# Optimization experiments

Hardware: AMD Instinct MI355X
Metric: run time of the kernel (lower is better)

Reference implementation:

```python
import jax, jax.numpy as jnp
import numpy as np

N = 50000
E = 800000
IN, HID, OUT = 20, 64, 2
HEADS, HD = 4, 64
EPS = 1e-5


def setup_inputs() -> dict:
    key = jax.random.key(0)
    ks = jax.random.split(key, 24)
    rn = lambda k, shape, s=0.1: (jax.random.normal(k, shape, dtype=jnp.float32) * s)
    inp = {}
    inp['x'] = jax.random.normal(ks[0], (N, IN), dtype=jnp.float32)
    inp['edge_index'] = jax.random.randint(ks[1], (2, E), 0, N, dtype=jnp.int64)
    # SAGEConv1: lin_l (aggregated msgs, bias), lin_r (root, no bias)
    inp['Wl1'] = rn(ks[2], (IN, HID)); inp['Wr1'] = rn(ks[3], (IN, HID)); inp['b1'] = jnp.zeros((HID,), jnp.float32)
    inp['g1'] = jnp.ones((HID,), jnp.float32); inp['bt1'] = jnp.zeros((HID,), jnp.float32)
    # GATConv: W2 projects to heads*dim; att vectors per head; bias size HID (concat=False)
    inp['W2'] = rn(ks[4], (HID, HEADS * HD)); inp['att_src'] = rn(ks[5], (HEADS, HD)); inp['att_dst'] = rn(ks[6], (HEADS, HD)); inp['b2'] = jnp.zeros((HID,), jnp.float32)
    inp['g2'] = jnp.ones((HID,), jnp.float32); inp['bt2'] = jnp.zeros((HID,), jnp.float32)
    # SAGEConv3: hidden -> hidden//2
    inp['Wl3'] = rn(ks[7], (HID, HID // 2)); inp['Wr3'] = rn(ks[8], (HID, HID // 2)); inp['b3'] = jnp.zeros((HID // 2,), jnp.float32)
    inp['g3'] = jnp.ones((HID // 2,), jnp.float32); inp['bt3'] = jnp.zeros((HID // 2,), jnp.float32)
    # skip + classifier
    inp['Wskip'] = rn(ks[9], (IN, HID // 2)); inp['bskip'] = jnp.zeros((HID // 2,), jnp.float32)
    inp['Wc1'] = rn(ks[10], (HID // 2, 32)); inp['bc1'] = jnp.zeros((32,), jnp.float32)
    inp['Wc2'] = rn(ks[11], (32, OUT)); inp['bc2'] = jnp.zeros((OUT,), jnp.float32)
    return inp


def _bn_eval(h, g, b):
    # eval-mode BatchNorm with freshly initialized running stats (mean=0, var=1)
    return h * (g / jnp.sqrt(1.0 + EPS)) + b


def reference(x, edge_index, Wl1, Wr1, b1, g1, bt1, W2, att_src, att_dst, b2, g2, bt2,
              Wl3, Wr3, b3, g3, bt3, Wskip, bskip, Wc1, bc1, Wc2, bc2):
    src, dst = edge_index[0], edge_index[1]
    deg = jnp.clip(jax.ops.segment_sum(jnp.ones((E,), x.dtype), dst, num_segments=N), 1.0)

    def sage(h, Wl, Wr, b):
        agg = jax.ops.segment_sum(h[src], dst, num_segments=N) / deg[:, None]  # mean aggregation
        return agg @ Wl + h @ Wr + b

    def gat(h):
        hp = (h @ W2).reshape(N, HEADS, HD)                    # [N,H,D]
        a_s = jnp.einsum('nhd,hd->nh', hp, att_src)            # [N,H]
        a_d = jnp.einsum('nhd,hd->nh', hp, att_dst)
        e = jax.nn.leaky_relu(a_s[src] + a_d[dst], 0.2)        # [E,H]
        m = jax.ops.segment_max(e, dst, num_segments=N)        # segment softmax over incoming edges
        ex = jnp.exp(e - m[dst])
        denom = jax.ops.segment_sum(ex, dst, num_segments=N)
        alpha = ex / (denom[dst] + 1e-16)                      # [E,H]
        out = jax.ops.segment_sum(hp[src] * alpha[:, :, None], dst, num_segments=N)  # [N,H,D]
        return out.mean(axis=1) + b2                            # concat=False -> mean over heads

    identity = x @ Wskip + bskip
    h = jax.nn.relu(_bn_eval(sage(x, Wl1, Wr1, b1), g1, bt1))   # dropout inactive (eval)
    h = jax.nn.relu(_bn_eval(gat(h), g2, bt2))
    h = jax.nn.relu(_bn_eval(sage(h, Wl3, Wr3, b3), g3, bt3))
    h = h + identity
    logits = jax.nn.relu(h @ Wc1 + bc1) @ Wc2 + bc2
    return jax.nn.log_softmax(logits, axis=1)
```

## Files before the change

### kernel.cpp

```cpp
#include <hip/hip_runtime.h>
#include <hip/hip_fp16.h>
#include <math.h>

#define NN 50000
#define NE 800000
#define IN_F 20
#define HID 64
#define HEADS 4
#define HD 64
#define CH 32
#define C1 32
#define OUTC 2

__global__ void k_scan_block(const int* __restrict__ in, int* __restrict__ out,
                             int* __restrict__ bsum, int n){
  __shared__ int tmp[256];
  int g = blockIdx.x * 256 + threadIdx.x;
  int v = (g < n) ? in[g] : 0;
  tmp[threadIdx.x] = v;
  __syncthreads();
  for (int o = 1; o < 256; o <<= 1) {
    int t = ((int)threadIdx.x >= o) ? tmp[threadIdx.x - o] : 0;
    __syncthreads();
    tmp[threadIdx.x] += t;
    __syncthreads();
  }
  if (g < n) out[g] = tmp[threadIdx.x] - v;
  if (bsum && threadIdx.x == 255) bsum[blockIdx.x] = tmp[255];
}

__global__ void k_add_off(int* __restrict__ rowptr, const int* __restrict__ bsum_ex, int n){
  int g = blockIdx.x * 256 + threadIdx.x;
  if (g < n) rowptr[g] += bsum_ex[g >> 8];
  if (g == 0) rowptr[NN] = NE;
}

__global__ void k_scatter(const int* __restrict__ src, const int* __restrict__ dst,
                          const int* __restrict__ rowptr, int* __restrict__ cnt2,
                          unsigned* __restrict__ colu){
  int e = blockIdx.x * 256 + threadIdx.x;
  if (e >= NE) return;
  int d = dst[e];
  int p = rowptr[d] + atomicAdd(&cnt2[d], 1);
  colu[p] = (unsigned)src[e] | ((unsigned)d << 16);
}

__global__ void k_prep(const float* __restrict__ x, const float* __restrict__ W2,
                       const float* __restrict__ att_src, const float* __restrict__ att_dst,
                       const int* __restrict__ dst,
                       __half* __restrict__ xh, float* __restrict__ was,
                       float* __restrict__ wad, float* __restrict__ W2r,
                       int* __restrict__ count){
  int i = blockIdx.x * 256 + threadIdx.x;
  if (i < NN * IN_F) xh[i] = __float2half(x[i]);
  if (i < NE) atomicAdd(&count[dst[i]], 1);
  if (i < 256 * 64) {
    int hk = i >> 6, d = i & 63;
    int h = hk >> 6, k = hk & 63;
    W2r[i] = W2[k * 256 + h * 64 + d];
  }
  if (i < 256) {
    int h = i >> 6, k = i & 63;
    float s = 0.f, dd = 0.f;
    for (int d = 0; d < 64; d++) {
      float w = W2[k * 256 + h * 64 + d];
      s  += w * att_src[h * 64 + d];
      dd += w * att_dst[h * 64 + d];
    }
    was[i] = s; wad[i] = dd;
  }
}

__global__ void k_aggx_gather(const int* __restrict__ rowptr, const unsigned* __restrict__ colu,
                              const __half* __restrict__ xh, float* __restrict__ aggx){
  int wid = threadIdx.x >> 6, lane = threadIdx.x & 63;
  int grp = lane >> 5, f = lane & 31;
  int n = blockIdx.x * 4 + wid;
  if (n >= NN) return;
  int r0 = rowptr[n], r1 = rowptr[n + 1];
  int mid = r0 + ((r1 - r0) >> 1);
  int jlo = grp ? mid : r0;
  int jhi = grp ? r1 : mid;
  int ff = f < IN_F ? f : 0;
  float acc = 0.f;
#define AX4(a,b,c,d) { \
    float v0 = __half2float(xh[(int)((a)&0xffffu) * IN_F + ff]); \
    float v1 = __half2float(xh[(int)((b)&0xffffu) * IN_F + ff]); \
    float v2 = __half2float(xh[(int)((c)&0xffffu) * IN_F + ff]); \
    float v3 = __half2float(xh[(int)((d)&0xffffu) * IN_F + ff]); \
    acc += (v0 + v1) + (v2 + v3); }
  int j = jlo;
  if (j + 4 <= jhi) {
    unsigned c0 = colu[j], c1 = colu[j+1], c2 = colu[j+2], c3 = colu[j+3];
    for (j += 4; j + 4 <= jhi; j += 4) {
      unsigned n0 = colu[j], n1 = colu[j+1], n2 = colu[j+2], n3 = colu[j+3];
      AX4(c0, c1, c2, c3);
      c0 = n0; c1 = n1; c2 = n2; c3 = n3;
    }
    AX4(c0, c1, c2, c3);
  }
  for (; j < jhi; j++) acc += __half2float(xh[(int)(colu[j] & 0xffffu) * IN_F + ff]);
#undef AX4
  acc += __shfl_xor(acc, 32);
  if (grp == 0 && f < IN_F) aggx[n * IN_F + f] = acc;
}

__global__ void k_sage1(const float* __restrict__ x, const float* __restrict__ aggx,
                        const int* __restrict__ count,
                        const float* __restrict__ Wl, const float* __restrict__ Wr,
                        const float* __restrict__ b, const float* __restrict__ g,
                        const float* __restrict__ bt,
                        const float* __restrict__ was, const float* __restrict__ wad,
                        __half* __restrict__ h1h, float* __restrict__ a_s,
                        float* __restrict__ a_d){
  __shared__ float sWl[IN_F * HID], sWr[IN_F * HID], sWas[256], sWad[256];
  for (int i = threadIdx.x; i < IN_F * HID; i += 256) { sWl[i] = Wl[i]; sWr[i] = Wr[i]; }
  { int i = threadIdx.x; sWas[i] = was[i]; sWad[i] = wad[i]; }
  __syncthreads();
  int idx = blockIdx.x * 256 + threadIdx.x;
  if (idx >= NN * HID) return;
  int n = idx >> 6, j = idx & 63;
  float inv = 1.f / fmaxf((float)count[n], 1.f);
  const float* xr = x + n * IN_F;
  const float* ar = aggx + n * IN_F;
  float acc = b[j];
  #pragma unroll
  for (int k = 0; k < IN_F; k++)
    acc += (ar[k] * inv) * sWl[k * HID + j] + xr[k] * sWr[k * HID + j];
  acc = acc * (g[j] * rsqrtf(1.f + 1e-5f)) + bt[j];
  acc = fmaxf(acc, 0.f);
  h1h[idx] = __float2half(acc);
  #pragma unroll
  for (int h = 0; h < HEADS; h++) {
    float vs = acc * sWas[h * 64 + j];
    float vd = acc * sWad[h * 64 + j];
    #pragma unroll
    for (int o = 32; o > 0; o >>= 1) { vs += __shfl_down(vs, o); vd += __shfl_down(vd, o); }
    if (j == 0) { a_s[n * 4 + h] = vs; a_d[n * 4 + h] = vd; }
  }
}

static __device__ __forceinline__ float4 edge_p(float4 as, float4 ad){
  float e0 = as.x + ad.x; e0 = e0 >= 0.f ? e0 : 0.2f * e0;
  float e1 = as.y + ad.y; e1 = e1 >= 0.f ? e1 : 0.2f * e1;
  float e2 = as.z + ad.z; e2 = e2 >= 0.f ? e2 : 0.2f * e2;
  float e3 = as.w + ad.w; e3 = e3 >= 0.f ? e3 : 0.2f * e3;
  return make_float4(__expf(e0), __expf(e1), __expf(e2), __expf(e3));
}

__global__ void k_gat_fused(const int* __restrict__ rowptr, const unsigned* __restrict__ colu,
                            const float4* __restrict__ a_s4, const float4* __restrict__ a_d4,
                            const __half* __restrict__ h1h, __half* __restrict__ z){
  int wid = threadIdx.x >> 6;
  int lane = threadIdx.x & 63;
  int grp = lane >> 5;
  int idx = lane & 31;
  int n = blockIdx.x * 4 + wid;
  if (n >= NN) return;
  int r0 = rowptr[n], r1 = rowptr[n + 1];
  int mid = r0 + ((r1 - r0) >> 1);
  int jlo = grp ? mid : r0;
  int jhi = grp ? r1 : mid;
  float4 ad = a_d4[n];
  float l0 = 0.f, l1 = 0.f, l2 = 0.f, l3 = 0.f;
  float2 ac0 = {0,0}, ac1 = {0,0}, ac2 = {0,0}, ac3 = {0,0};
#define GAT1(cc) { \
    int s = (int)((cc) & 0xffffu); \
    float4 as = a_s4[s]; \
    float2 v = __half22float2(*(const __half2*)(h1h + (size_t)s * 64 + 2 * idx)); \
    float4 p = edge_p(as, ad); \
    l0 += p.x; l1 += p.y; l2 += p.z; l3 += p.w; \
    ac0.x += p.x*v.x; ac0.y += p.x*v.y; \
    ac1.x += p.y*v.x; ac1.y += p.y*v.y; \
    ac2.x += p.z*v.x; ac2.y += p.z*v.y; \
    ac3.x += p.w*v.x; ac3.y += p.w*v.y; }
#define GAT4(q0,q1,q2,q3) { \
    int s0=(int)((q0)&0xffffu), s1=(int)((q1)&0xffffu), s2=(int)((q2)&0xffffu), s3=(int)((q3)&0xffffu); \
    float4 as0 = a_s4[s0], as1 = a_s4[s1], as2 = a_s4[s2], as3 = a_s4[s3]; \
    float2 v0 = __half22float2(*(const __half2*)(h1h + (size_t)s0 * 64 + 2 * idx)); \
    float2 v1 = __half22float2(*(const __half2*)(h1h + (size_t)s1 * 64 + 2 * idx)); \
    float2 v2 = __half22float2(*(const __half2*)(h1h + (size_t)s2 * 64 + 2 * idx)); \
    float2 v3 = __half22float2(*(const __half2*)(h1h + (size_t)s3 * 64 + 2 * idx)); \
    float4 p0 = edge_p(as0, ad), p1 = edge_p(as1, ad); \
    float4 p2 = edge_p(as2, ad), p3 = edge_p(as3, ad); \
    l0 += (p0.x + p1.x) + (p2.x + p3.x); \
    l1 += (p0.y + p1.y) + (p2.y + p3.y); \
    l2 += (p0.z + p1.z) + (p2.z + p3.z); \
    l3 += (p0.w + p1.w) + (p2.w + p3.w); \
    ac0.x += p0.x*v0.x + p1.x*v1.x + p2.x*v2.x + p3.x*v3.x; \
    ac0.y += p0.x*v0.y + p1.x*v1.y + p2.x*v2.y + p3.x*v3.y; \
    ac1.x += p0.y*v0.x + p1.y*v1.x + p2.y*v2.x + p3.y*v3.x; \
    ac1.y += p0.y*v0.y + p1.y*v1.y + p2.y*v2.y + p3.y*v3.y; \
    ac2.x += p0.z*v0.x + p1.z*v1.x + p2.z*v2.x + p3.z*v3.x; \
    ac2.y += p0.z*v0.y + p1.z*v1.y + p2.z*v2.y + p3.z*v3.y; \
    ac3.x += p0.w*v0.x + p1.w*v1.x + p2.w*v2.x + p3.w*v3.x; \
    ac3.y += p0.w*v0.y + p1.w*v1.y + p2.w*v2.y + p3.w*v3.y; }
  int j = jlo;
  if (j + 4 <= jhi) {
    unsigned c0 = colu[j], c1 = colu[j+1], c2 = colu[j+2], c3 = colu[j+3];
    for (j += 4; j + 4 <= jhi; j += 4) {
      unsigned n0 = colu[j], n1 = colu[j+1], n2 = colu[j+2], n3 = colu[j+3];
      GAT4(c0, c1, c2, c3);
      c0 = n0; c1 = n1; c2 = n2; c3 = n3;
    }
    GAT4(c0, c1, c2, c3);
  }
  for (; j < jhi; j++) { unsigned cc = colu[j]; GAT1(cc); }
#undef GAT4
#undef GAT1
  l0 += __shfl_xor(l0, 32); l1 += __shfl_xor(l1, 32);
  l2 += __shfl_xor(l2, 32); l3 += __shfl_xor(l3, 32);
  ac0.x += __shfl_xor(ac0.x, 32); ac0.y += __shfl_xor(ac0.y, 32);
  ac1.x += __shfl_xor(ac1.x, 32); ac1.y += __shfl_xor(ac1.y, 32);
  ac2.x += __shfl_xor(ac2.x, 32); ac2.y += __shfl_xor(ac2.y, 32);
  ac3.x += __shfl_xor(ac3.x, 32); ac3.y += __shfl_xor(ac3.y, 32);
  if (grp == 0) {
    float i0 = 1.f / (4.f * (l0 + 1e-16f));
    float i1 = 1.f / (4.f * (l1 + 1e-16f));
    float i2 = 1.f / (4.f * (l2 + 1e-16f));
    float i3 = 1.f / (4.f * (l3 + 1e-16f));
    __half* zr = z + (size_t)n * 256;
    *(__half2*)(zr +       2 * idx) = __floats2half2_rn(ac0.x * i0, ac0.y * i0);
    *(__half2*)(zr +  64 + 2 * idx) = __floats2half2_rn(ac1.x * i1, ac1.y * i1);
    *(__half2*)(zr + 128 + 2 * idx) = __floats2half2_rn(ac2.x * i2, ac2.y * i2);
    *(__half2*)(zr + 192 + 2 * idx) = __floats2half2_rn(ac3.x * i3, ac3.y * i3);
  }
}

__global__ void __launch_bounds__(256) k_zproj(const __half* __restrict__ z,
                      const float* __restrict__ W2r, const float* __restrict__ b2,
                      const float* __restrict__ g2, const float* __restrict__ bt2,
                      __half* __restrict__ h2h){
  __shared__ float sz[4][256];
  __shared__ float sacc[4][4][64];
  int tid = threadIdx.x;
  int w = tid >> 6, d = tid & 63;
  float wreg[64];
  #pragma unroll
  for (int i = 0; i < 64; i++) wreg[i] = W2r[(w * 64 + i) * 64 + d];
  float gd = g2[d] * rsqrtf(1.f + 1e-5f), btd = bt2[d], bd = b2[d];
  int n0base = blockIdx.x * 64;
  for (int r = 0; r < 16; r++) {
    int n0 = n0base + r * 4;
    for (int i = tid; i < 512; i += 256) {
      int m = i >> 7, c = (i & 127) * 2;
      int n = n0 + m;
      if (n < NN) {
        __half2 hv = *(const __half2*)(z + (size_t)n * 256 + c);
        float2 f = __half22float2(hv);
        sz[m][c] = f.x; sz[m][c + 1] = f.y;
      } else { sz[m][c] = 0.f; sz[m][c + 1] = 0.f; }
    }
    __syncthreads();
    #pragma unroll
    for (int m = 0; m < 4; m++) {
      float acc = 0.f;
      #pragma unroll
      for (int i = 0; i < 64; i++) acc += sz[m][w * 64 + i] * wreg[i];
      sacc[m][w][d] = acc;
    }
    __syncthreads();
    int n = n0 + w;
    if (n < NN) {
      float rr = sacc[w][0][d] + sacc[w][1][d] + sacc[w][2][d] + sacc[w][3][d] + bd;
      rr = rr * gd + btd;
      rr = fmaxf(rr, 0.f);
      h2h[(size_t)n * 64 + d] = __float2half(rr);
    }
    __syncthreads();
  }
}

__global__ void __launch_bounds__(256) k_sage3f(
    const int* __restrict__ rowptr, const unsigned* __restrict__ colu,
    const __half* __restrict__ h2h, const int* __restrict__ count,
    const float* __restrict__ Wl3, const float* __restrict__ Wr3,
    const float* __restrict__ b3, const float* __restrict__ g3,
    const float* __restrict__ bt3, float* __restrict__ h3){
  __shared__ float sWl[HID * CH], sWr[HID * CH];
  __shared__ float sA[4][HID], sH[4][HID];
  for (int i = threadIdx.x; i < HID * CH; i += 256) { sWl[i] = Wl3[i]; sWr[i] = Wr3[i]; }
  int wid = threadIdx.x >> 6, lane = threadIdx.x & 63;
  int grp = lane >> 5, idx = lane & 31;
  int n = blockIdx.x * 4 + wid;
  int nc = n < NN ? n : NN - 1;
  int r0 = rowptr[nc], r1 = rowptr[nc + 1];
  int mid = r0 + ((r1 - r0) >> 1);
  int jlo = grp ? mid : r0;
  int jhi = grp ? r1 : mid;
  float2 av = {0, 0};
#define AGG4(q0,q1,q2,q3) { \
    int s0=(int)((q0)&0xffffu), s1=(int)((q1)&0xffffu), s2=(int)((q2)&0xffffu), s3=(int)((q3)&0xffffu); \
    float2 v0 = __half22float2(*(const __half2*)(h2h + (size_t)s0 * 64 + 2 * idx)); \
    float2 v1 = __half22float2(*(const __half2*)(h2h + (size_t)s1 * 64 + 2 * idx)); \
    float2 v2 = __half22float2(*(const __half2*)(h2h + (size_t)s2 * 64 + 2 * idx)); \
    float2 v3 = __half22float2(*(const __half2*)(h2h + (size_t)s3 * 64 + 2 * idx)); \
    av.x += (v0.x + v1.x) + (v2.x + v3.x); \
    av.y += (v0.y + v1.y) + (v2.y + v3.y); }
  int j = jlo;
  if (j + 4 <= jhi) {
    unsigned c0 = colu[j], c1 = colu[j+1], c2 = colu[j+2], c3 = colu[j+3];
    for (j += 4; j + 4 <= jhi; j += 4) {
      unsigned n0 = colu[j], n1 = colu[j+1], n2 = colu[j+2], n3 = colu[j+3];
      AGG4(c0, c1, c2, c3);
      c0 = n0; c1 = n1; c2 = n2; c3 = n3;
    }
    AGG4(c0, c1, c2, c3);
  }
  for (; j < jhi; j++) {
    float2 v = __half22float2(*(const __half2*)(h2h + (size_t)(colu[j] & 0xffffu) * 64 + 2 * idx));
    av.x += v.x; av.y += v.y;
  }
#undef AGG4
  av.x += __shfl_xor(av.x, 32);
  av.y += __shfl_xor(av.y, 32);
  float inv = 1.f / fmaxf((float)count[nc], 1.f);
  if (grp == 0) { sA[wid][2 * idx] = av.x * inv; sA[wid][2 * idx + 1] = av.y * inv; }
  sH[wid][lane] = __half2float(h2h[(size_t)nc * 64 + lane]);
  __syncthreads();
  int kbase = grp * 32;
  float c0 = 0.f, c1 = 0.f;
  #pragma unroll
  for (int k0 = 0; k0 < 32; k0 += 2) {
    int k = kbase + k0;
    c0 += sA[wid][k] * sWl[k * CH + idx] + sH[wid][k] * sWr[k * CH + idx];
    c1 += sA[wid][k+1] * sWl[(k+1) * CH + idx] + sH[wid][k+1] * sWr[(k+1) * CH + idx];
  }
  float c = c0 + c1;
  c += __shfl_xor(c, 32);
  if (grp == 0 && n < NN) {
    float acc = c + b3[idx];
    acc = acc * (g3[idx] * rsqrtf(1.f + 1e-5f)) + bt3[idx];
    h3[(size_t)n * CH + idx] = fmaxf(acc, 0.f);
  }
}

__global__ void __launch_bounds__(256) k_cls(const float* __restrict__ h3,
                      const float* __restrict__ x,
                      const float* __restrict__ Wskip, const float* __restrict__ bskip,
                      const float* __restrict__ Wc1, const float* __restrict__ bc1,
                      const float* __restrict__ Wc2, const float* __restrict__ bc2,
                      float* __restrict__ out){
  __shared__ float sW1[C1 * C1], sW2[C1 * OUTC], sb1[C1], sb2[OUTC];
  __shared__ float sWs[IN_F * CH], sbsk[CH];
  __shared__ float sh3[256][CH + 1];
  int tid = threadIdx.x;
  int n0 = blockIdx.x * 256;
  for (int i = tid; i < C1 * C1; i += 256) sW1[i] = Wc1[i];
  for (int i = tid; i < IN_F * CH; i += 256) sWs[i] = Wskip[i];
  if (tid < C1 * OUTC) sW2[tid] = Wc2[tid];
  if (tid < C1) { sb1[tid] = bc1[tid]; sbsk[tid] = bskip[tid]; }
  if (tid < OUTC) sb2[tid] = bc2[tid];
  for (int i = tid; i < 256 * CH; i += 256) {
    int m = i >> 5, c = i & 31;
    int n = n0 + m;
    sh3[m][c] = (n < NN) ? h3[(size_t)n * CH + c] : 0.f;
  }
  __syncthreads();
  int n = n0 + tid;
  if (n >= NN) return;
  float xr[IN_F];
  #pragma unroll
  for (int k = 0; k < IN_F; k++) xr[k] = x[(size_t)n * IN_F + k];
  float hrow[CH];
  #pragma unroll
  for (int j = 0; j < CH; j++) {
    float idn = sbsk[j];
    #pragma unroll
    for (int k = 0; k < IN_F; k++) idn += xr[k] * sWs[k * CH + j];
    hrow[j] = sh3[tid][j] + idn;
  }
  float l0 = sb2[0], l1 = sb2[1];
  #pragma unroll
  for (int i = 0; i < C1; i++) {
    float c0 = sb1[i], c1 = 0.f;
    #pragma unroll
    for (int j = 0; j < CH; j += 2) {
      c0 += hrow[j] * sW1[j * C1 + i];
      c1 += hrow[j + 1] * sW1[(j + 1) * C1 + i];
    }
    float c = fmaxf(c0 + c1, 0.f);
    l0 += c * sW2[i * OUTC + 0];
    l1 += c * sW2[i * OUTC + 1];
  }
  float mx = fmaxf(l0, l1);
  float lse = mx + logf(expf(l0 - mx) + expf(l1 - mx));
  out[n * OUTC + 0] = l0 - lse;
  out[n * OUTC + 1] = l1 - lse;
}

extern "C" void kernel_launch(void* const* d_in, const int* in_sizes, int n_in,
                              void* d_out, int out_size, void* d_ws, size_t ws_size,
                              hipStream_t stream) {
  const float* x       = (const float*)d_in[0];
  const int*   ei      = (const int*)d_in[1];
  const float* Wl1     = (const float*)d_in[2];
  const float* Wr1     = (const float*)d_in[3];
  const float* b1      = (const float*)d_in[4];
  const float* g1      = (const float*)d_in[5];
  const float* bt1     = (const float*)d_in[6];
  const float* W2      = (const float*)d_in[7];
  const float* att_src = (const float*)d_in[8];
  const float* att_dst = (const float*)d_in[9];
  const float* b2      = (const float*)d_in[10];
  const float* g2      = (const float*)d_in[11];
  const float* bt2     = (const float*)d_in[12];
  const float* Wl3     = (const float*)d_in[13];
  const float* Wr3     = (const float*)d_in[14];
  const float* b3      = (const float*)d_in[15];
  const float* g3      = (const float*)d_in[16];
  const float* bt3     = (const float*)d_in[17];
  const float* Wskip   = (const float*)d_in[18];
  const float* bskip   = (const float*)d_in[19];
  const float* Wc1     = (const float*)d_in[20];
  const float* bc1     = (const float*)d_in[21];
  const float* Wc2     = (const float*)d_in[22];
  const float* bc2     = (const float*)d_in[23];
  float* out = (float*)d_out;

  const int* src = ei;
  const int* dst = ei + NE;

  float* ws = (float*)d_ws;
  size_t off = 0;
  auto alloc = [&](size_t nf) { size_t o = off; off += (nf + 63) & ~(size_t)63; return o; };
  size_t o_count = alloc(NN);
  size_t o_cnt2  = alloc(NN);
  size_t zero_elems = off;
  size_t o_rowptr = alloc(NN + 1);
  size_t o_bsum   = alloc(256);
  size_t o_bsumex = alloc(256);
  size_t o_colu   = alloc(NE);
  size_t o_xh     = alloc((size_t)NN * IN_F / 2 + 64);
  size_t o_aggx   = alloc((size_t)NN * IN_F);
  size_t o_h1h    = alloc((size_t)NN * HID / 2 + 64);
  size_t o_as     = alloc((size_t)NN * HEADS);
  size_t o_ad     = alloc((size_t)NN * HEADS);
  size_t o_was    = alloc(256);
  size_t o_wad    = alloc(256);
  size_t o_w2r    = alloc(256 * 64);
  size_t o_z      = alloc((size_t)NN * 256 / 2 + 64);
  size_t o_h2h    = alloc((size_t)NN * HID / 2 + 64);
  size_t o_h3     = alloc((size_t)NN * CH);
  (void)ws_size; (void)in_sizes; (void)n_in; (void)out_size;

  int* count     = (int*)(ws + o_count);
  int* cnt2      = (int*)(ws + o_cnt2);
  int* rowptr    = (int*)(ws + o_rowptr);
  int* bsum      = (int*)(ws + o_bsum);
  int* bsumex    = (int*)(ws + o_bsumex);
  unsigned* colu = (unsigned*)(ws + o_colu);
  __half* xh     = (__half*)(ws + o_xh);
  float* aggx    = ws + o_aggx;
  __half* h1h    = (__half*)(ws + o_h1h);
  float* a_s     = ws + o_as;
  float* a_d     = ws + o_ad;
  float* was     = ws + o_was;
  float* wad     = ws + o_wad;
  float* W2r     = ws + o_w2r;
  __half* z      = (__half*)(ws + o_z);
  __half* h2h    = (__half*)(ws + o_h2h);
  float* h3      = ws + o_h3;

  auto nb = [](long long n) { return (int)((n + 255) / 256); };
  const int nscan = nb(NN);

  hipMemsetAsync(ws, 0, zero_elems * sizeof(int), stream);
  k_prep<<<nb((long long)NN * IN_F), 256, 0, stream>>>(x, W2, att_src, att_dst, dst,
                                                       xh, was, wad, W2r, count);
  k_scan_block<<<nscan, 256, 0, stream>>>(count, rowptr, bsum, NN);
  k_scan_block<<<1, 256, 0, stream>>>(bsum, bsumex, nullptr, nscan);
  k_add_off<<<nscan, 256, 0, stream>>>(rowptr, bsumex, NN);
  k_scatter<<<nb(NE), 256, 0, stream>>>(src, dst, rowptr, cnt2, colu);
  k_aggx_gather<<<(NN + 3) / 4, 256, 0, stream>>>(rowptr, colu, xh, aggx);
  k_sage1<<<nb((long long)NN * HID), 256, 0, stream>>>(x, aggx, count, Wl1, Wr1, b1, g1, bt1,
                                                       was, wad, h1h, a_s, a_d);
  k_gat_fused<<<(NN + 3) / 4, 256, 0, stream>>>(rowptr, colu, (const float4*)a_s,
                                                (const float4*)a_d, h1h, z);
  k_zproj<<<(NN + 63) / 64, 256, 0, stream>>>(z, W2r, b2, g2, bt2, h2h);
  k_sage3f<<<(NN + 3) / 4, 256, 0, stream>>>(rowptr, colu, h2h, count,
                                             Wl3, Wr3, b3, g3, bt3, h3);
  k_cls<<<(NN + 255) / 256, 256, 0, stream>>>(h3, x, Wskip, bskip, Wc1, bc1, Wc2, bc2, out);
}
```

Before: 309.9 us.

## Fuse SAGE1 gather with its transform and SAGE3 with classifier; drop cnt2

Merges the neighbor-feature gather into the first SAGE layer so each node's wave does both the aggregation and the 20x64 projection via shuffles, removing the aggx buffer and one launch. The third SAGE layer now also computes the skip path, the classifier MLP and log-softmax in-warp, eliminating the h3 buffer and the k_cls kernel. The scatter bumps rowptr entries atomically, so afterwards each entry holds its row end and kernels read the start from the previous entry; this drops the separate cnt2 counter. The trade-off is more per-wave shuffle work and more shared-memory staging per block in the fused kernels.

```diff
diff --git a/kernel.cpp b/kernel.cpp
--- a/kernel.cpp
+++ b/kernel.cpp
@@ -32,16 +32,14 @@
 __global__ void k_add_off(int* __restrict__ rowptr, const int* __restrict__ bsum_ex, int n){
   int g = blockIdx.x * 256 + threadIdx.x;
   if (g < n) rowptr[g] += bsum_ex[g >> 8];
-  if (g == 0) rowptr[NN] = NE;
 }
 
 __global__ void k_scatter(const int* __restrict__ src, const int* __restrict__ dst,
-                          const int* __restrict__ rowptr, int* __restrict__ cnt2,
-                          unsigned* __restrict__ colu){
+                          int* __restrict__ rowptrM, unsigned* __restrict__ colu){
   int e = blockIdx.x * 256 + threadIdx.x;
   if (e >= NE) return;
   int d = dst[e];
-  int p = rowptr[d] + atomicAdd(&cnt2[d], 1);
+  int p = atomicAdd(&rowptrM[d], 1);
   colu[p] = (unsigned)src[e] | ((unsigned)d << 16);
 }
 
@@ -71,21 +69,33 @@
   }
 }
 
-__global__ void k_aggx_gather(const int* __restrict__ rowptr, const unsigned* __restrict__ colu,
-                              const __half* __restrict__ xh, float* __restrict__ aggx){
+__global__ void __launch_bounds__(256) k_sage1f(
+    const int* __restrict__ rowptrM, const unsigned* __restrict__ colu,
+    const float* __restrict__ x, const __half* __restrict__ xh,
+    const int* __restrict__ count,
+    const float* __restrict__ Wl, const float* __restrict__ Wr,
+    const float* __restrict__ b, const float* __restrict__ g,
+    const float* __restrict__ bt,
+    const float* __restrict__ was, const float* __restrict__ wad,
+    __half* __restrict__ h1h, float* __restrict__ a_s, float* __restrict__ a_d){
+  __shared__ float sWl[IN_F * HID], sWr[IN_F * HID], sWas[256], sWad[256];
+  for (int i = threadIdx.x; i < IN_F * HID; i += 256) { sWl[i] = Wl[i]; sWr[i] = Wr[i]; }
+  { int i = threadIdx.x; sWas[i] = was[i]; sWad[i] = wad[i]; }
+  __syncthreads();
   int wid = threadIdx.x >> 6, lane = threadIdx.x & 63;
   int grp = lane >> 5, f = lane & 31;
   int n = blockIdx.x * 4 + wid;
   if (n >= NN) return;
-  int r0 = rowptr[n], r1 = rowptr[n + 1];
+  int r1 = rowptrM[n];
+  int r0 = n ? rowptrM[n - 1] : 0;
   int mid = r0 + ((r1 - r0) >> 1);
   int jlo = grp ? mid : r0;
   int jhi = grp ? r1 : mid;
   int ff = f < IN_F ? f : 0;
   float acc = 0.f;
-#define AX4(a,b,c,d) { \
+#define AX4(a,b_,c,d) { \
     float v0 = __half2float(xh[(int)((a)&0xffffu) * IN_F + ff]); \
-    float v1 = __half2float(xh[(int)((b)&0xffffu) * IN_F + ff]); \
+    float v1 = __half2float(xh[(int)((b_)&0xffffu) * IN_F + ff]); \
     float v2 = __half2float(xh[(int)((c)&0xffffu) * IN_F + ff]); \
     float v3 = __half2float(xh[(int)((d)&0xffffu) * IN_F + ff]); \
     acc += (v0 + v1) + (v2 + v3); }
@@ -102,41 +112,25 @@
   for (; j < jhi; j++) acc += __half2float(xh[(int)(colu[j] & 0xffffu) * IN_F + ff]);
 #undef AX4
   acc += __shfl_xor(acc, 32);
-  if (grp == 0 && f < IN_F) aggx[n * IN_F + f] = acc;
-}
-
-__global__ void k_sage1(const float* __restrict__ x, const float* __restrict__ aggx,
-                        const int* __restrict__ count,
-                        const float* __restrict__ Wl, const float* __restrict__ Wr,
-                        const float* __restrict__ b, const float* __restrict__ g,
-                        const float* __restrict__ bt,
-                        const float* __restrict__ was, const float* __restrict__ wad,
-                        __half* __restrict__ h1h, float* __restrict__ a_s,
-                        float* __restrict__ a_d){
-  __shared__ float sWl[IN_F * HID], sWr[IN_F * HID], sWas[256], sWad[256];
-  for (int i = threadIdx.x; i < IN_F * HID; i += 256) { sWl[i] = Wl[i]; sWr[i] = Wr[i]; }
-  { int i = threadIdx.x; sWas[i] = was[i]; sWad[i] = wad[i]; }
-  __syncthreads();
-  int idx = blockIdx.x * 256 + threadIdx.x;
-  if (idx >= NN * HID) return;
-  int n = idx >> 6, j = idx & 63;
   float inv = 1.f / fmaxf((float)count[n], 1.f);
-  const float* xr = x + n * IN_F;
-  const float* ar = aggx + n * IN_F;
-  float acc = b[j];
-  #pragma unroll
-  for (int k = 0; k < IN_F; k++)
-    acc += (ar[k] * inv) * sWl[k * HID + j] + xr[k] * sWr[k * HID + j];
-  acc = acc * (g[j] * rsqrtf(1.f + 1e-5f)) + bt[j];
-  acc = fmaxf(acc, 0.f);
-  h1h[idx] = __float2half(acc);
-  #pragma unroll
-  for (int h = 0; h < HEADS; h++) {
-    float vs = acc * sWas[h * 64 + j];
-    float vd = acc * sWad[h * 64 + j];
+  float xv = (f < IN_F) ? x[(size_t)n * IN_F + ff] : 0.f;
+  float h = b[lane];
+  #pragma unroll
+  for (int k = 0; k < IN_F; k++) {
+    float aggk = __shfl(acc, k);
+    float xk = __shfl(xv, k);
+    h += (aggk * inv) * sWl[k * HID + lane] + xk * sWr[k * HID + lane];
+  }
+  h = h * (g[lane] * rsqrtf(1.f + 1e-5f)) + bt[lane];
+  h = fmaxf(h, 0.f);
+  h1h[(size_t)n * HID + lane] = __float2half(h);
+  #pragma unroll
+  for (int hh = 0; hh < HEADS; hh++) {
+    float vs = h * sWas[hh * 64 + lane];
+    float vd = h * sWad[hh * 64 + lane];
     #pragma unroll
     for (int o = 32; o > 0; o >>= 1) { vs += __shfl_down(vs, o); vd += __shfl_down(vd, o); }
-    if (j == 0) { a_s[n * 4 + h] = vs; a_d[n * 4 + h] = vd; }
+    if (lane == 0) { a_s[n * 4 + hh] = vs; a_d[n * 4 + hh] = vd; }
   }
 }
 
@@ -148,7 +142,7 @@
   return make_float4(__expf(e0), __expf(e1), __expf(e2), __expf(e3));
 }
 
-__global__ void k_gat_fused(const int* __restrict__ rowptr, const unsigned* __restrict__ colu,
+__global__ void k_gat_fused(const int* __restrict__ rowptrM, const unsigned* __restrict__ colu,
                             const float4* __restrict__ a_s4, const float4* __restrict__ a_d4,
                             const __half* __restrict__ h1h, __half* __restrict__ z){
   int wid = threadIdx.x >> 6;
@@ -157,7 +151,8 @@
   int idx = lane & 31;
   int n = blockIdx.x * 4 + wid;
   if (n >= NN) return;
-  int r0 = rowptr[n], r1 = rowptr[n + 1];
+  int r1 = rowptrM[n];
+  int r0 = n ? rowptrM[n - 1] : 0;
   int mid = r0 + ((r1 - r0) >> 1);
   int jlo = grp ? mid : r0;
   int jhi = grp ? r1 : mid;
@@ -271,20 +266,30 @@
   }
 }
 
-__global__ void __launch_bounds__(256) k_sage3f(
-    const int* __restrict__ rowptr, const unsigned* __restrict__ colu,
+__global__ void __launch_bounds__(256) k_sage3c(
+    const int* __restrict__ rowptrM, const unsigned* __restrict__ colu,
     const __half* __restrict__ h2h, const int* __restrict__ count,
+    const float* __restrict__ x,
     const float* __restrict__ Wl3, const float* __restrict__ Wr3,
     const float* __restrict__ b3, const float* __restrict__ g3,
-    const float* __restrict__ bt3, float* __restrict__ h3){
-  __shared__ float sWl[HID * CH], sWr[HID * CH];
+    const float* __restrict__ bt3,
+    const float* __restrict__ Wskip, const float* __restrict__ bskip,
+    const float* __restrict__ Wc1, const float* __restrict__ bc1,
+    const float* __restrict__ Wc2, const float* __restrict__ bc2,
+    float* __restrict__ out){
+  __shared__ float sWl[HID * CH], sWr[HID * CH], sWs[IN_F * CH];
+  __shared__ float sW1[C1 * C1], sW2[C1 * OUTC];
   __shared__ float sA[4][HID], sH[4][HID];
   for (int i = threadIdx.x; i < HID * CH; i += 256) { sWl[i] = Wl3[i]; sWr[i] = Wr3[i]; }
+  for (int i = threadIdx.x; i < IN_F * CH; i += 256) sWs[i] = Wskip[i];
+  for (int i = threadIdx.x; i < C1 * C1; i += 256) sW1[i] = Wc1[i];
+  if (threadIdx.x < C1 * OUTC) sW2[threadIdx.x] = Wc2[threadIdx.x];
   int wid = threadIdx.x >> 6, lane = threadIdx.x & 63;
   int grp = lane >> 5, idx = lane & 31;
   int n = blockIdx.x * 4 + wid;
   int nc = n < NN ? n : NN - 1;
-  int r0 = rowptr[nc], r1 = rowptr[nc + 1];
+  int r1 = rowptrM[nc];
+  int r0 = nc ? rowptrM[nc - 1] : 0;
   int mid = r0 + ((r1 - r0) >> 1);
   int jlo = grp ? mid : r0;
   int jhi = grp ? r1 : mid;
@@ -328,65 +333,29 @@
   }
   float c = c0 + c1;
   c += __shfl_xor(c, 32);
-  if (grp == 0 && n < NN) {
-    float acc = c + b3[idx];
-    acc = acc * (g3[idx] * rsqrtf(1.f + 1e-5f)) + bt3[idx];
-    h3[(size_t)n * CH + idx] = fmaxf(acc, 0.f);
-  }
-}
-
-__global__ void __launch_bounds__(256) k_cls(const float* __restrict__ h3,
-                      const float* __restrict__ x,
-                      const float* __restrict__ Wskip, const float* __restrict__ bskip,
-                      const float* __restrict__ Wc1, const float* __restrict__ bc1,
-                      const float* __restrict__ Wc2, const float* __restrict__ bc2,
-                      float* __restrict__ out){
-  __shared__ float sW1[C1 * C1], sW2[C1 * OUTC], sb1[C1], sb2[OUTC];
-  __shared__ float sWs[IN_F * CH], sbsk[CH];
-  __shared__ float sh3[256][CH + 1];
-  int tid = threadIdx.x;
-  int n0 = blockIdx.x * 256;
-  for (int i = tid; i < C1 * C1; i += 256) sW1[i] = Wc1[i];
-  for (int i = tid; i < IN_F * CH; i += 256) sWs[i] = Wskip[i];
-  if (tid < C1 * OUTC) sW2[tid] = Wc2[tid];
-  if (tid < C1) { sb1[tid] = bc1[tid]; sbsk[tid] = bskip[tid]; }
-  if (tid < OUTC) sb2[tid] = bc2[tid];
-  for (int i = tid; i < 256 * CH; i += 256) {
-    int m = i >> 5, c = i & 31;
-    int n = n0 + m;
-    sh3[m][c] = (n < NN) ? h3[(size_t)n * CH + c] : 0.f;
-  }
-  __syncthreads();
-  int n = n0 + tid;
-  if (n >= NN) return;
-  float xr[IN_F];
-  #pragma unroll
-  for (int k = 0; k < IN_F; k++) xr[k] = x[(size_t)n * IN_F + k];
-  float hrow[CH];
-  #pragma unroll
-  for (int j = 0; j < CH; j++) {
-    float idn = sbsk[j];
-    #pragma unroll
-    for (int k = 0; k < IN_F; k++) idn += xr[k] * sWs[k * CH + j];
-    hrow[j] = sh3[tid][j] + idn;
-  }
-  float l0 = sb2[0], l1 = sb2[1];
-  #pragma unroll
-  for (int i = 0; i < C1; i++) {
-    float c0 = sb1[i], c1 = 0.f;
-    #pragma unroll
-    for (int j = 0; j < CH; j += 2) {
-      c0 += hrow[j] * sW1[j * C1 + i];
-      c1 += hrow[j + 1] * sW1[(j + 1) * C1 + i];
-    }
-    float c = fmaxf(c0 + c1, 0.f);
-    l0 += c * sW2[i * OUTC + 0];
-    l1 += c * sW2[i * OUTC + 1];
-  }
-  float mx = fmaxf(l0, l1);
-  float lse = mx + logf(expf(l0 - mx) + expf(l1 - mx));
-  out[n * OUTC + 0] = l0 - lse;
-  out[n * OUTC + 1] = l1 - lse;
+  float xv = (idx < IN_F) ? x[(size_t)nc * IN_F + idx] : 0.f;
+  float bnv = c + b3[idx];
+  bnv = bnv * (g3[idx] * rsqrtf(1.f + 1e-5f)) + bt3[idx];
+  bnv = fmaxf(bnv, 0.f);
+  float idn = bskip[idx];
+  #pragma unroll
+  for (int k = 0; k < IN_F; k++) idn += __shfl(xv, k) * sWs[k * CH + idx];
+  float hrow = bnv + idn;
+  float ci = bc1[idx];
+  #pragma unroll
+  for (int jj = 0; jj < CH; jj++) ci += __shfl(hrow, jj) * sW1[jj * C1 + idx];
+  ci = fmaxf(ci, 0.f);
+  float p0 = ci * sW2[idx * OUTC + 0];
+  float p1 = ci * sW2[idx * OUTC + 1];
+  #pragma unroll
+  for (int o = 16; o > 0; o >>= 1) { p0 += __shfl_xor(p0, o); p1 += __shfl_xor(p1, o); }
+  if (lane == 0 && n < NN) {
+    float l0 = p0 + bc2[0], l1 = p1 + bc2[1];
+    float mx = fmaxf(l0, l1);
+    float lse = mx + logf(expf(l0 - mx) + expf(l1 - mx));
+    out[(size_t)n * OUTC + 0] = l0 - lse;
+    out[(size_t)n * OUTC + 1] = l1 - lse;
+  }
 }
 
 extern "C" void kernel_launch(void* const* d_in, const int* in_sizes, int n_in,
@@ -425,14 +394,12 @@
   size_t off = 0;
   auto alloc = [&](size_t nf) { size_t o = off; off += (nf + 63) & ~(size_t)63; return o; };
   size_t o_count = alloc(NN);
-  size_t o_cnt2  = alloc(NN);
   size_t zero_elems = off;
   size_t o_rowptr = alloc(NN + 1);
   size_t o_bsum   = alloc(256);
   size_t o_bsumex = alloc(256);
   size_t o_colu   = alloc(NE);
   size_t o_xh     = alloc((size_t)NN * IN_F / 2 + 64);
-  size_t o_aggx   = alloc((size_t)NN * IN_F);
   size_t o_h1h    = alloc((size_t)NN * HID / 2 + 64);
   size_t o_as     = alloc((size_t)NN * HEADS);
   size_t o_ad     = alloc((size_t)NN * HEADS);
@@ -441,17 +408,14 @@
   size_t o_w2r    = alloc(256 * 64);
   size_t o_z      = alloc((size_t)NN * 256 / 2 + 64);
   size_t o_h2h    = alloc((size_t)NN * HID / 2 + 64);
-  size_t o_h3     = alloc((size_t)NN * CH);
   (void)ws_size; (void)in_sizes; (void)n_in; (void)out_size;
 
   int* count     = (int*)(ws + o_count);
-  int* cnt2      = (int*)(ws + o_cnt2);
   int* rowptr    = (int*)(ws + o_rowptr);
   int* bsum      = (int*)(ws + o_bsum);
   int* bsumex    = (int*)(ws + o_bsumex);
   unsigned* colu = (unsigned*)(ws + o_colu);
   __half* xh     = (__half*)(ws + o_xh);
-  float* aggx    = ws + o_aggx;
   __half* h1h    = (__half*)(ws + o_h1h);
   float* a_s     = ws + o_as;
   float* a_d     = ws + o_ad;
@@ -460,7 +424,6 @@
   float* W2r     = ws + o_w2r;
   __half* z      = (__half*)(ws + o_z);
   __half* h2h    = (__half*)(ws + o_h2h);
-  float* h3      = ws + o_h3;
 
   auto nb = [](long long n) { return (int)((n + 255) / 256); };
   const int nscan = nb(NN);
@@ -471,14 +434,14 @@
   k_scan_block<<<nscan, 256, 0, stream>>>(count, rowptr, bsum, NN);
   k_scan_block<<<1, 256, 0, stream>>>(bsum, bsumex, nullptr, nscan);
   k_add_off<<<nscan, 256, 0, stream>>>(rowptr, bsumex, NN);
-  k_scatter<<<nb(NE), 256, 0, stream>>>(src, dst, rowptr, cnt2, colu);
-  k_aggx_gather<<<(NN + 3) / 4, 256, 0, stream>>>(rowptr, colu, xh, aggx);
-  k_sage1<<<nb((long long)NN * HID), 256, 0, stream>>>(x, aggx, count, Wl1, Wr1, b1, g1, bt1,
-                                                       was, wad, h1h, a_s, a_d);
+  k_scatter<<<nb(NE), 256, 0, stream>>>(src, dst, rowptr, colu);
+  k_sage1f<<<(NN + 3) / 4, 256, 0, stream>>>(rowptr, colu, x, xh, count,
+                                             Wl1, Wr1, b1, g1, bt1, was, wad,
+                                             h1h, a_s, a_d);
   k_gat_fused<<<(NN + 3) / 4, 256, 0, stream>>>(rowptr, colu, (const float4*)a_s,
                                                 (const float4*)a_d, h1h, z);
   k_zproj<<<(NN + 63) / 64, 256, 0, stream>>>(z, W2r, b2, g2, bt2, h2h);
-  k_sage3f<<<(NN + 3) / 4, 256, 0, stream>>>(rowptr, colu, h2h, count,
-                                             Wl3, Wr3, b3, g3, bt3, h3);
-  k_cls<<<(NN + 255) / 256, 256, 0, stream>>>(h3, x, Wskip, bskip, Wc1, bc1, Wc2, bc2, out);
-}
+  k_sage3c<<<(NN + 3) / 4, 256, 0, stream>>>(rowptr, colu, h2h, count, x,
+                                             Wl3, Wr3, b3, g3, bt3,
+                                             Wskip, bskip, Wc1, bc1, Wc2, bc2, out);
+}
```

After: 355.3 us. +14.6%, slower.

## Fuse SAGE1 gather with linear layer and scatter in-place on rowptr

Applied to the files above, without the earlier changes.

The first-layer neighbor aggregation is merged with the SAGE1 linear, batch-norm and attention-logit computation into one wavefront-per-node kernel. Aggregated features are broadcast across lanes with shuffles instead of being written to and re-read from an aggx buffer. The scatter now bumps rowptr itself, so after scattering rowptr[n] holds the end of row n. All consumers read start as rowptr[n-1] and derive the degree from the row length, which removes the cnt2 and count reads. The cost is one extra kernel launch removed and less global traffic, while the sage1 linear now runs per node with a serial shuffle loop.

```diff
diff --git a/kernel.cpp b/kernel.cpp
--- a/kernel.cpp
+++ b/kernel.cpp
@@ -32,16 +32,14 @@
 __global__ void k_add_off(int* __restrict__ rowptr, const int* __restrict__ bsum_ex, int n){
   int g = blockIdx.x * 256 + threadIdx.x;
   if (g < n) rowptr[g] += bsum_ex[g >> 8];
-  if (g == 0) rowptr[NN] = NE;
 }
 
 __global__ void k_scatter(const int* __restrict__ src, const int* __restrict__ dst,
-                          const int* __restrict__ rowptr, int* __restrict__ cnt2,
-                          unsigned* __restrict__ colu){
+                          int* __restrict__ rowptrM, unsigned* __restrict__ colu){
   int e = blockIdx.x * 256 + threadIdx.x;
   if (e >= NE) return;
   int d = dst[e];
-  int p = rowptr[d] + atomicAdd(&cnt2[d], 1);
+  int p = atomicAdd(&rowptrM[d], 1);
   colu[p] = (unsigned)src[e] | ((unsigned)d << 16);
 }
 
@@ -71,21 +69,32 @@
   }
 }
 
-__global__ void k_aggx_gather(const int* __restrict__ rowptr, const unsigned* __restrict__ colu,
-                              const __half* __restrict__ xh, float* __restrict__ aggx){
+__global__ void __launch_bounds__(256) k_sage1f(
+    const int* __restrict__ rowptrM, const unsigned* __restrict__ colu,
+    const float* __restrict__ x, const __half* __restrict__ xh,
+    const float* __restrict__ Wl, const float* __restrict__ Wr,
+    const float* __restrict__ b, const float* __restrict__ g,
+    const float* __restrict__ bt,
+    const float* __restrict__ was, const float* __restrict__ wad,
+    __half* __restrict__ h1h, float* __restrict__ a_s, float* __restrict__ a_d){
+  __shared__ float sWl[IN_F * HID], sWr[IN_F * HID], sWas[256], sWad[256];
+  for (int i = threadIdx.x; i < IN_F * HID; i += 256) { sWl[i] = Wl[i]; sWr[i] = Wr[i]; }
+  { int i = threadIdx.x; sWas[i] = was[i]; sWad[i] = wad[i]; }
+  __syncthreads();
   int wid = threadIdx.x >> 6, lane = threadIdx.x & 63;
   int grp = lane >> 5, f = lane & 31;
   int n = blockIdx.x * 4 + wid;
   if (n >= NN) return;
-  int r0 = rowptr[n], r1 = rowptr[n + 1];
+  int r1 = rowptrM[n];
+  int r0 = n ? rowptrM[n - 1] : 0;
   int mid = r0 + ((r1 - r0) >> 1);
   int jlo = grp ? mid : r0;
   int jhi = grp ? r1 : mid;
   int ff = f < IN_F ? f : 0;
   float acc = 0.f;
-#define AX4(a,b,c,d) { \
+#define AX4(a,b_,c,d) { \
     float v0 = __half2float(xh[(int)((a)&0xffffu) * IN_F + ff]); \
-    float v1 = __half2float(xh[(int)((b)&0xffffu) * IN_F + ff]); \
+    float v1 = __half2float(xh[(int)((b_)&0xffffu) * IN_F + ff]); \
     float v2 = __half2float(xh[(int)((c)&0xffffu) * IN_F + ff]); \
     float v3 = __half2float(xh[(int)((d)&0xffffu) * IN_F + ff]); \
     acc += (v0 + v1) + (v2 + v3); }
@@ -102,41 +111,25 @@
   for (; j < jhi; j++) acc += __half2float(xh[(int)(colu[j] & 0xffffu) * IN_F + ff]);
 #undef AX4
   acc += __shfl_xor(acc, 32);
-  if (grp == 0 && f < IN_F) aggx[n * IN_F + f] = acc;
-}
-
-__global__ void k_sage1(const float* __restrict__ x, const float* __restrict__ aggx,
-                        const int* __restrict__ count,
-                        const float* __restrict__ Wl, const float* __restrict__ Wr,
-                        const float* __restrict__ b, const float* __restrict__ g,
-                        const float* __restrict__ bt,
-                        const float* __restrict__ was, const float* __restrict__ wad,
-                        __half* __restrict__ h1h, float* __restrict__ a_s,
-                        float* __restrict__ a_d){
-  __shared__ float sWl[IN_F * HID], sWr[IN_F * HID], sWas[256], sWad[256];
-  for (int i = threadIdx.x; i < IN_F * HID; i += 256) { sWl[i] = Wl[i]; sWr[i] = Wr[i]; }
-  { int i = threadIdx.x; sWas[i] = was[i]; sWad[i] = wad[i]; }
-  __syncthreads();
-  int idx = blockIdx.x * 256 + threadIdx.x;
-  if (idx >= NN * HID) return;
-  int n = idx >> 6, j = idx & 63;
-  float inv = 1.f / fmaxf((float)count[n], 1.f);
-  const float* xr = x + n * IN_F;
-  const float* ar = aggx + n * IN_F;
-  float acc = b[j];
-  #pragma unroll
-  for (int k = 0; k < IN_F; k++)
-    acc += (ar[k] * inv) * sWl[k * HID + j] + xr[k] * sWr[k * HID + j];
-  acc = acc * (g[j] * rsqrtf(1.f + 1e-5f)) + bt[j];
-  acc = fmaxf(acc, 0.f);
-  h1h[idx] = __float2half(acc);
-  #pragma unroll
-  for (int h = 0; h < HEADS; h++) {
-    float vs = acc * sWas[h * 64 + j];
-    float vd = acc * sWad[h * 64 + j];
+  float inv = 1.f / fmaxf((float)(r1 - r0), 1.f);
+  float xv = (f < IN_F) ? x[(size_t)n * IN_F + ff] : 0.f;
+  float h = b[lane];
+  #pragma unroll
+  for (int k = 0; k < IN_F; k++) {
+    float aggk = __shfl(acc, k);
+    float xk = __shfl(xv, k);
+    h += (aggk * inv) * sWl[k * HID + lane] + xk * sWr[k * HID + lane];
+  }
+  h = h * (g[lane] * rsqrtf(1.f + 1e-5f)) + bt[lane];
+  h = fmaxf(h, 0.f);
+  h1h[(size_t)n * HID + lane] = __float2half(h);
+  #pragma unroll
+  for (int hh = 0; hh < HEADS; hh++) {
+    float vs = h * sWas[hh * 64 + lane];
+    float vd = h * sWad[hh * 64 + lane];
     #pragma unroll
     for (int o = 32; o > 0; o >>= 1) { vs += __shfl_down(vs, o); vd += __shfl_down(vd, o); }
-    if (j == 0) { a_s[n * 4 + h] = vs; a_d[n * 4 + h] = vd; }
+    if (lane == 0) { a_s[n * 4 + hh] = vs; a_d[n * 4 + hh] = vd; }
   }
 }
 
@@ -148,7 +141,7 @@
   return make_float4(__expf(e0), __expf(e1), __expf(e2), __expf(e3));
 }
 
-__global__ void k_gat_fused(const int* __restrict__ rowptr, const unsigned* __restrict__ colu,
+__global__ void k_gat_fused(const int* __restrict__ rowptrM, const unsigned* __restrict__ colu,
                             const float4* __restrict__ a_s4, const float4* __restrict__ a_d4,
                             const __half* __restrict__ h1h, __half* __restrict__ z){
   int wid = threadIdx.x >> 6;
@@ -157,7 +150,8 @@
   int idx = lane & 31;
   int n = blockIdx.x * 4 + wid;
   if (n >= NN) return;
-  int r0 = rowptr[n], r1 = rowptr[n + 1];
+  int r1 = rowptrM[n];
+  int r0 = n ? rowptrM[n - 1] : 0;
   int mid = r0 + ((r1 - r0) >> 1);
   int jlo = grp ? mid : r0;
   int jhi = grp ? r1 : mid;
@@ -272,8 +266,8 @@
 }
 
 __global__ void __launch_bounds__(256) k_sage3f(
-    const int* __restrict__ rowptr, const unsigned* __restrict__ colu,
-    const __half* __restrict__ h2h, const int* __restrict__ count,
+    const int* __restrict__ rowptrM, const unsigned* __restrict__ colu,
+    const __half* __restrict__ h2h,
     const float* __restrict__ Wl3, const float* __restrict__ Wr3,
     const float* __restrict__ b3, const float* __restrict__ g3,
     const float* __restrict__ bt3, float* __restrict__ h3){
@@ -284,7 +278,8 @@
   int grp = lane >> 5, idx = lane & 31;
   int n = blockIdx.x * 4 + wid;
   int nc = n < NN ? n : NN - 1;
-  int r0 = rowptr[nc], r1 = rowptr[nc + 1];
+  int r1 = rowptrM[nc];
+  int r0 = nc ? rowptrM[nc - 1] : 0;
   int mid = r0 + ((r1 - r0) >> 1);
   int jlo = grp ? mid : r0;
   int jhi = grp ? r1 : mid;
@@ -314,7 +309,7 @@
 #undef AGG4
   av.x += __shfl_xor(av.x, 32);
   av.y += __shfl_xor(av.y, 32);
-  float inv = 1.f / fmaxf((float)count[nc], 1.f);
+  float inv = 1.f / fmaxf((float)(r1 - r0), 1.f);
   if (grp == 0) { sA[wid][2 * idx] = av.x * inv; sA[wid][2 * idx + 1] = av.y * inv; }
   sH[wid][lane] = __half2float(h2h[(size_t)nc * 64 + lane]);
   __syncthreads();
@@ -425,14 +420,12 @@
   size_t off = 0;
   auto alloc = [&](size_t nf) { size_t o = off; off += (nf + 63) & ~(size_t)63; return o; };
   size_t o_count = alloc(NN);
-  size_t o_cnt2  = alloc(NN);
   size_t zero_elems = off;
   size_t o_rowptr = alloc(NN + 1);
   size_t o_bsum   = alloc(256);
   size_t o_bsumex = alloc(256);
   size_t o_colu   = alloc(NE);
   size_t o_xh     = alloc((size_t)NN * IN_F / 2 + 64);
-  size_t o_aggx   = alloc((size_t)NN * IN_F);
   size_t o_h1h    = alloc((size_t)NN * HID / 2 + 64);
   size_t o_as     = alloc((size_t)NN * HEADS);
   size_t o_ad     = alloc((size_t)NN * HEADS);
@@ -445,13 +438,11 @@
   (void)ws_size; (void)in_sizes; (void)n_in; (void)out_size;
 
   int* count     = (int*)(ws + o_count);
-  int* cnt2      = (int*)(ws + o_cnt2);
   int* rowptr    = (int*)(ws + o_rowptr);
   int* bsum      = (int*)(ws + o_bsum);
   int* bsumex    = (int*)(ws + o_bsumex);
   unsigned* colu = (unsigned*)(ws + o_colu);
   __half* xh     = (__half*)(ws + o_xh);
-  float* aggx    = ws + o_aggx;
   __half* h1h    = (__half*)(ws + o_h1h);
   float* a_s     = ws + o_as;
   float* a_d     = ws + o_ad;
@@ -471,14 +462,14 @@
   k_scan_block<<<nscan, 256, 0, stream>>>(count, rowptr, bsum, NN);
   k_scan_block<<<1, 256, 0, stream>>>(bsum, bsumex, nullptr, nscan);
   k_add_off<<<nscan, 256, 0, stream>>>(rowptr, bsumex, NN);
-  k_scatter<<<nb(NE), 256, 0, stream>>>(src, dst, rowptr, cnt2, colu);
-  k_aggx_gather<<<(NN + 3) / 4, 256, 0, stream>>>(rowptr, colu, xh, aggx);
-  k_sage1<<<nb((long long)NN * HID), 256, 0, stream>>>(x, aggx, count, Wl1, Wr1, b1, g1, bt1,
-                                                       was, wad, h1h, a_s, a_d);
+  k_scatter<<<nb(NE), 256, 0, stream>>>(src, dst, rowptr, colu);
+  k_sage1f<<<(NN + 3) / 4, 256, 0, stream>>>(rowptr, colu, x, xh,
+                                             Wl1, Wr1, b1, g1, bt1, was, wad,
+                                             h1h, a_s, a_d);
   k_gat_fused<<<(NN + 3) / 4, 256, 0, stream>>>(rowptr, colu, (const float4*)a_s,
                                                 (const float4*)a_d, h1h, z);
   k_zproj<<<(NN + 63) / 64, 256, 0, stream>>>(z, W2r, b2, g2, bt2, h2h);
-  k_sage3f<<<(NN + 3) / 4, 256, 0, stream>>>(rowptr, colu, h2h, count,
+  k_sage3f<<<(NN + 3) / 4, 256, 0, stream>>>(rowptr, colu, h2h,
                                              Wl3, Wr3, b3, g3, bt3, h3);
   k_cls<<<(NN + 255) / 256, 256, 0, stream>>>(h3, x, Wskip, bskip, Wc1, bc1, Wc2, bc2, out);
 }
```

Result: slower. 320.7 us (+3.5%).
